# Kernel tuning notes

Hardware: AMD Instinct MI355X
Metric: run time of the kernel (lower is better)

Reference implementation:

```python
import jax, jax.numpy as jnp
import numpy as np

M_POS = 0.5
M_NEG_SIM = 0.1
LAM_NEG = 1.0


def setup_inputs() -> dict:
    key = jax.random.key(0)
    N, d, G = 8192, 1024, 64
    codebook = jax.random.normal(key, (N, d), dtype=jnp.float32)
    base = (jnp.arange(N) // G) * G  # contiguous groups of size G (vq_to_range)
    starts = base.astype(jnp.int32)
    ends = (base + G - 1).astype(jnp.int32)
    return {"codebook": codebook, "starts": starts, "ends": ends, "max_i": N - 1}


def reference(codebook, starts, ends, max_i):
    N, d = codebook.shape
    M = min(N, int(max_i) + 1)  # rows processed by the python loop

    # cosine similarity rows [0:M] vs all N
    zn = codebook / jnp.linalg.norm(codebook, axis=-1, keepdims=True)
    cos = jnp.einsum('md,nd->mn', zn[:M], zn)  # (M, N)

    # pairwise Euclidean distances rows [0:M] vs all N via ||a-b||^2 = |a|^2+|b|^2-2ab
    sq = jnp.sum(codebook * codebook, axis=-1)  # (N,)
    dot = jnp.einsum('md,nd->mn', codebook[:M], codebook)  # (M, N)
    d2 = jnp.maximum(sq[:M, None] + sq[None, :] - 2.0 * dot, 0.0)

    j = jnp.arange(N)[None, :]
    i = jnp.arange(M)[:, None]
    in_range = (j >= starts[:M, None]) & (j <= ends[:M, None])
    pos_mask = in_range & (j != i)
    # original: group_mask[i]=False then neg = ~group_mask, so i is in negatives
    neg_mask = (~in_range) | (j == i)

    pos_cnt = jnp.sum(pos_mask, axis=-1)
    neg_cnt = jnp.sum(neg_mask, axis=-1)

    # safe sqrt: only evaluate on positive-mask entries
    D = jnp.sqrt(jnp.where(pos_mask, d2, 1.0))
    pos_term = jnp.square(jax.nn.relu(D - M_POS)) * pos_mask
    pos_pull = jnp.sum(pos_term, axis=-1) / jnp.maximum(pos_cnt, 1)

    neg_cos = jnp.clip(cos, -1.0, 1.0)
    neg_term = jnp.square(jax.nn.relu(jnp.abs(neg_cos) - M_NEG_SIM)) * neg_mask
    ortho = jnp.sum(neg_term, axis=-1) / jnp.maximum(neg_cnt, 1)

    valid = (pos_cnt > 0) & (neg_cnt > 0)
    per_row = jnp.where(valid, pos_pull + LAM_NEG * ortho, 0.0)
    cnt = jnp.sum(valid)
    total = jnp.sum(per_row)
    return jnp.where(cnt > 0, total / jnp.maximum(cnt, 1).astype(total.dtype), jnp.zeros((), total.dtype))
```

## Files before the change

### kernel.cpp

```cpp
#include <hip/hip_runtime.h>
#include <hip/hip_bf16.h>
#include <stdint.h>

#define M_POS 0.5f
#define M_NEG 0.1f
#define LAM_NEG 1.0f

typedef __attribute__((ext_vector_type(4))) float floatx4;
typedef __attribute__((ext_vector_type(8))) int   intx8;
typedef __attribute__((ext_vector_type(4))) int   int32x4;

union Frag8 { intx8 v; int4 q[2]; };

__global__ __launch_bounds__(256) void prep_kernel(
    const float* __restrict__ cb, unsigned char* __restrict__ cb_q,
    float* __restrict__ sq, float* __restrict__ inv_norm,
    unsigned* __restrict__ zero_base, int zero_len,
    int N, int d)
{
    const int gi = blockIdx.x * 256 + threadIdx.x;
    if (gi < zero_len) zero_base[gi] = 0u;

    const int t = threadIdx.x;
    const int w = t >> 6, l = t & 63;
    const int row = blockIdx.x * 4 + w;
    if (row >= N) return;
    const float* src = cb + (size_t)row * d;
    unsigned char* dst = cb_q + (size_t)row * d;

    float s = 0.f;
    for (int c = l * 16; c < d; c += 1024) {
        float4 v0 = *(const float4*)(src + c);
        float4 v1 = *(const float4*)(src + c + 4);
        float4 v2 = *(const float4*)(src + c + 8);
        float4 v3 = *(const float4*)(src + c + 12);
        s += v0.x*v0.x + v0.y*v0.y + v0.z*v0.z + v0.w*v0.w
           + v1.x*v1.x + v1.y*v1.y + v1.z*v1.z + v1.w*v1.w
           + v2.x*v2.x + v2.y*v2.y + v2.z*v2.z + v2.w*v2.w
           + v3.x*v3.x + v3.y*v3.y + v3.z*v3.z + v3.w*v3.w;
        int p0 = __builtin_amdgcn_cvt_pk_fp8_f32(v0.x, v0.y, 0, false);
        p0     = __builtin_amdgcn_cvt_pk_fp8_f32(v0.z, v0.w, p0, true);
        int p1 = __builtin_amdgcn_cvt_pk_fp8_f32(v1.x, v1.y, 0, false);
        p1     = __builtin_amdgcn_cvt_pk_fp8_f32(v1.z, v1.w, p1, true);
        int p2 = __builtin_amdgcn_cvt_pk_fp8_f32(v2.x, v2.y, 0, false);
        p2     = __builtin_amdgcn_cvt_pk_fp8_f32(v2.z, v2.w, p2, true);
        int p3 = __builtin_amdgcn_cvt_pk_fp8_f32(v3.x, v3.y, 0, false);
        p3     = __builtin_amdgcn_cvt_pk_fp8_f32(v3.z, v3.w, p3, true);
        int32x4 pk; pk.x = p0; pk.y = p1; pk.z = p2; pk.w = p3;
        *(int32x4*)(dst + c) = pk;
    }
    for (int o = 32; o > 0; o >>= 1) s += __shfl_down(s, o, 64);
    if (l == 0) { sq[row] = s; inv_norm[row] = rsqrtf(s); }
}

__global__ __launch_bounds__(512, 1) void gram_loss_kernel(
    const unsigned char* __restrict__ A,
    const float* __restrict__ sq, const float* __restrict__ inv_norm,
    const int* __restrict__ starts, const int* __restrict__ ends,
    const int* __restrict__ max_ip,
    float* __restrict__ pos_acc, float* __restrict__ neg_acc,
    unsigned* __restrict__ counter, float* __restrict__ out,
    int N, int d)
{
    const int M = min(N, max_ip[0] + 1);

    int vt = blockIdx.x;
    const int nB = gridDim.x;
    if ((nB & 7) == 0) {
        const int per = nB >> 3;
        vt = (blockIdx.x & 7) * per + (blockIdx.x >> 3);
    }

    int bx = (int)((sqrtf(8.f * (float)vt + 1.f) - 1.f) * 0.5f);
    while ((bx + 1) * (bx + 2) / 2 <= vt) bx++;
    while (bx * (bx + 1) / 2 > vt) bx--;
    const int by = vt - bx * (bx + 1) / 2;

    const int rowBase = by * 256;
    const int colBase = bx * 256;
    const bool isDiag = (by == bx);

    __shared__ alignas(16) unsigned char ldsA[2][256 * 128];
    __shared__ alignas(16) unsigned char ldsB[2][256 * 128];

    const int tid  = threadIdx.x;
    const int wave = tid >> 6;
    const int lane = tid & 63;
    const int wr = (wave >> 2) * 128;
    const int wc = (wave & 3) * 64;

    floatx4 acc[8][4];
#pragma unroll
    for (int a = 0; a < 8; ++a)
#pragma unroll
        for (int b = 0; b < 4; ++b) acc[a][b] = (floatx4){0.f, 0.f, 0.f, 0.f};

    const int sRow8 = tid >> 3;
    const int sChk  = tid & 7;
    const int srcOffC = ((sChk ^ (sRow8 & 7)) * 16);
    const int kTiles = d / 128;

    const int rl = lane & 15;
    const int g  = lane >> 4;
    const int rx = rl & 7;
    const int c0 = (((2 * g)     ^ rx) * 16);
    const int c1 = (((2 * g + 1) ^ rx) * 16);

#define STAGE(SLOT, KT)                                                         \
    { const int k0_ = (KT) * 128;                                               \
      _Pragma("unroll")                                                         \
      for (int h = 0; h < 4; ++h) {                                             \
        const int r_ = h * 64 + sRow8;                                          \
        const unsigned char* ga_ = A + (size_t)(rowBase + r_) * d + k0_ + srcOffC; \
        const unsigned char* gb_ = A + (size_t)(colBase + r_) * d + k0_ + srcOffC; \
        __builtin_amdgcn_global_load_lds(                                       \
            (const __attribute__((address_space(1))) void*)ga_,                 \
            (__attribute__((address_space(3))) void*)(ldsA[SLOT] + r_ * 128 + sChk * 16), 16, 0, 0); \
        __builtin_amdgcn_global_load_lds(                                       \
            (const __attribute__((address_space(1))) void*)gb_,                 \
            (__attribute__((address_space(3))) void*)(ldsB[SLOT] + r_ * 128 + sChk * 16), 16, 0, 0); \
      } }

#define WAITV(NN)  asm volatile("s_waitcnt vmcnt(" #NN ")" ::: "memory")

    if (kTiles == 8) {
        STAGE(0, 0)
        __builtin_amdgcn_sched_barrier(0);
        STAGE(1, 1)
        __builtin_amdgcn_sched_barrier(0);
#pragma unroll
        for (int kt = 0; kt < 8; ++kt) {
            const int cur = kt & 1;
            if (kt < 7) { WAITV(8); } else { WAITV(0); }
            __builtin_amdgcn_s_barrier();

            Frag8 bfr[4];
#pragma unroll
            for (int ct = 0; ct < 4; ++ct) {
                const unsigned char* pb = ldsB[cur] + (wc + ct * 16 + rl) * 128;
                bfr[ct].q[0] = *(const int4*)(pb + c0);
                bfr[ct].q[1] = *(const int4*)(pb + c1);
            }
#pragma unroll
            for (int ph = 0; ph < 4; ++ph) {
                Frag8 af0, af1;
                const unsigned char* pa0 = ldsA[cur] + (wr + (2 * ph) * 16 + rl) * 128;
                const unsigned char* pa1 = ldsA[cur] + (wr + (2 * ph + 1) * 16 + rl) * 128;
                af0.q[0] = *(const int4*)(pa0 + c0);
                af0.q[1] = *(const int4*)(pa0 + c1);
                af1.q[0] = *(const int4*)(pa1 + c0);
                af1.q[1] = *(const int4*)(pa1 + c1);
                __builtin_amdgcn_s_setprio(1);
#pragma unroll
                for (int ct = 0; ct < 4; ++ct)
                    acc[2 * ph][ct] = __builtin_amdgcn_mfma_scale_f32_16x16x128_f8f6f4(
                        af0.v, bfr[ct].v, acc[2 * ph][ct], 0, 0, 0, 127, 0, 127);
#pragma unroll
                for (int ct = 0; ct < 4; ++ct)
                    acc[2 * ph + 1][ct] = __builtin_amdgcn_mfma_scale_f32_16x16x128_f8f6f4(
                        af1.v, bfr[ct].v, acc[2 * ph + 1][ct], 0, 0, 0, 127, 0, 127);
                __builtin_amdgcn_s_setprio(0);
                __builtin_amdgcn_sched_barrier(0);
            }

            __builtin_amdgcn_s_barrier();
            if (kt + 2 < 8) {
                STAGE(cur, kt + 2)
                __builtin_amdgcn_sched_barrier(0);
            }
        }
    } else {
        for (int kt = 0; kt < kTiles; ++kt) {
            STAGE(0, kt)
            WAITV(0);
            __builtin_amdgcn_s_barrier();
            Frag8 bfr[4];
#pragma unroll
            for (int ct = 0; ct < 4; ++ct) {
                const unsigned char* pb = ldsB[0] + (wc + ct * 16 + rl) * 128;
                bfr[ct].q[0] = *(const int4*)(pb + c0);
                bfr[ct].q[1] = *(const int4*)(pb + c1);
            }
#pragma unroll
            for (int rt = 0; rt < 8; ++rt) {
                Frag8 af;
                const unsigned char* pa = ldsA[0] + (wr + rt * 16 + rl) * 128;
                af.q[0] = *(const int4*)(pa + c0);
                af.q[1] = *(const int4*)(pa + c1);
#pragma unroll
                for (int ct = 0; ct < 4; ++ct)
                    acc[rt][ct] = __builtin_amdgcn_mfma_scale_f32_16x16x128_f8f6f4(
                        af.v, bfr[ct].v, acc[rt][ct], 0, 0, 0, 127, 0, 127);
            }
            __syncthreads();
        }
    }
#undef STAGE
#undef WAITV

    const int q  = lane >> 4;
    const int jlo = colBase + wc;
    const int ilo = rowBase + wr;

    int   jn[4];
    float jinv[4];
    bool  jvalid[4];
#pragma unroll
    for (int ct = 0; ct < 4; ++ct) {
        const int j = jlo + ct * 16 + rl;
        jn[ct]  = j;
        jinv[ct] = inv_norm[j];
        jvalid[ct] = (j < M);
    }

    bool posLane = false;
    {
        const int ri0 = ilo + lane;
        const int ri1 = ilo + 64 + lane;
        if (ri0 < M) posLane |= (ends[ri0] >= jlo) && (starts[ri0] <= jlo + 63);
        if (ri1 < M) posLane |= (ends[ri1] >= jlo) && (starts[ri1] <= jlo + 63);
        if (!isDiag) {
            const int cj = jlo + lane;
            if (cj < M) posLane |= (ends[cj] >= ilo) && (starts[cj] <= ilo + 127);
        }
    }
    const bool fullPath = (__ballot(posLane) != 0ULL);

    float posc[4] = {0.f, 0.f, 0.f, 0.f};
    float negc[4] = {0.f, 0.f, 0.f, 0.f};

    if (fullPath) {
        int   jns[4], jne[4];
        float jsq[4];
#pragma unroll
        for (int ct = 0; ct < 4; ++ct) {
            jsq[ct] = sq[jn[ct]];
            jns[ct] = jvalid[ct] ? starts[jn[ct]] : 0;
            jne[ct] = jvalid[ct] ? ends[jn[ct]]   : -1;
        }
#pragma unroll
        for (int rt = 0; rt < 8; ++rt) {
            const int ibase = ilo + rt * 16 + q * 4;
#pragma unroll
            for (int reg = 0; reg < 4; ++reg) {
                const int i = ibase + reg;
                const bool rowValid = (i < M);
                const int ns = rowValid ? starts[i] : 0;
                const int ne = rowValid ? ends[i]   : -1;
                const float iinv = inv_norm[i];
                const float isq  = sq[i];
                float posp = 0.f, negp = 0.f;
#pragma unroll
                for (int ct = 0; ct < 4; ++ct) {
                    const float dot = acc[rt][ct][reg];
                    const int j = jn[ct];
                    float cosv = dot * iinv * jinv[ct];
                    cosv = fminf(fmaxf(cosv, -1.f), 1.f);
                    float tn = fmaxf(fabsf(cosv) - M_NEG, 0.f);
                    const float nterm = tn * tn;
                    const float d2 = fmaxf(isq + jsq[ct] - 2.f * dot, 0.f);
                    float tp = fmaxf(sqrtf(d2) - M_POS, 0.f);
                    const float pterm = tp * tp;
                    const bool dg = (j == i);
                    if (rowValid) {
                        const bool in_r = (j >= ns) && (j <= ne);
                        if (in_r && !dg) posp += pterm;
                        if (!in_r || dg) negp += nterm;
                    }
                    if (!isDiag && jvalid[ct]) {
                        const bool in_c = (i >= jns[ct]) && (i <= jne[ct]);
                        if (in_c && !dg) posc[ct] += pterm;
                        if (!in_c || dg) negc[ct] += nterm;
                    }
                }
#pragma unroll
                for (int m = 1; m < 16; m <<= 1) {
                    posp += __shfl_xor(posp, m, 64);
                    negp += __shfl_xor(negp, m, 64);
                }
                if (rowValid && rl == 0) {
                    atomicAdd(&pos_acc[i], posp);
                    atomicAdd(&neg_acc[i], negp);
                }
            }
        }
        if (!isDiag) {
#pragma unroll
            for (int ct = 0; ct < 4; ++ct) {
                posc[ct] += __shfl_xor(posc[ct], 16, 64);
                posc[ct] += __shfl_xor(posc[ct], 32, 64);
                negc[ct] += __shfl_xor(negc[ct], 16, 64);
                negc[ct] += __shfl_xor(negc[ct], 32, 64);
            }
            if (q == 0) {
#pragma unroll
                for (int ct = 0; ct < 4; ++ct) {
                    if (jvalid[ct]) {
                        atomicAdd(&pos_acc[jn[ct]], posc[ct]);
                        atomicAdd(&neg_acc[jn[ct]], negc[ct]);
                    }
                }
            }
        }
    } else {
#pragma unroll
        for (int rt = 0; rt < 8; ++rt) {
            const int ibase = ilo + rt * 16 + q * 4;
#pragma unroll
            for (int reg = 0; reg < 4; ++reg) {
                const int i = ibase + reg;
                const float iinv = inv_norm[i];
                float negp = 0.f;
#pragma unroll
                for (int ct = 0; ct < 4; ++ct) {
                    const float dot = acc[rt][ct][reg];
                    float cosv = dot * iinv * jinv[ct];
                    cosv = fminf(fmaxf(cosv, -1.f), 1.f);
                    float tn = fmaxf(fabsf(cosv) - M_NEG, 0.f);
                    const float nterm = tn * tn;
                    negp += nterm;
                    negc[ct] += nterm;
                }
#pragma unroll
                for (int m = 1; m < 16; m <<= 1)
                    negp += __shfl_xor(negp, m, 64);
                if ((i < M) && rl == 0)
                    atomicAdd(&neg_acc[i], negp);
            }
        }
        if (!isDiag) {
#pragma unroll
            for (int ct = 0; ct < 4; ++ct) {
                negc[ct] += __shfl_xor(negc[ct], 16, 64);
                negc[ct] += __shfl_xor(negc[ct], 32, 64);
            }
            if (q == 0) {
#pragma unroll
                for (int ct = 0; ct < 4; ++ct)
                    if (jvalid[ct])
                        atomicAdd(&neg_acc[jn[ct]], negc[ct]);
            }
        }
    }

    struct FinSm { int amLast; float ts[8]; int cs[8]; };
    FinSm* fs = (FinSm*)&ldsA[0][0];
    __syncthreads();
    if (tid == 0) {
        __threadfence();
        unsigned old = atomicAdd(counter, 1u);
        fs->amLast = (old == (unsigned)(gridDim.x - 1)) ? 1 : 0;
    }
    __syncthreads();
    if (fs->amLast) {
        __threadfence();
        float total = 0.f;
        int cnt = 0;
        for (int i = tid; i < M; i += 512) {
            const float pa = __hip_atomic_load(&pos_acc[i], __ATOMIC_RELAXED, __HIP_MEMORY_SCOPE_AGENT);
            const float na = __hip_atomic_load(&neg_acc[i], __ATOMIC_RELAXED, __HIP_MEMORY_SCOPE_AGENT);
            const int ns = starts[i], ne = ends[i];
            const int lo = max(ns, 0), hi = min(ne, N - 1);
            const int inr = max(hi - lo + 1, 0);
            const bool dg = (i >= ns) && (i <= ne);
            const int pos_cnt = inr - (dg ? 1 : 0);
            const int neg_cnt = N - inr + (dg ? 1 : 0);
            if (pos_cnt > 0 && neg_cnt > 0) {
                total += pa / (float)max(pos_cnt, 1)
                       + LAM_NEG * na / (float)max(neg_cnt, 1);
                cnt++;
            }
        }
        for (int o = 32; o > 0; o >>= 1) {
            total += __shfl_down(total, o, 64);
            cnt   += __shfl_down(cnt, o, 64);
        }
        if (lane == 0) { fs->ts[wave] = total; fs->cs[wave] = cnt; }
        __syncthreads();
        if (tid == 0) {
            float T = 0.f; int C = 0;
            for (int wv = 0; wv < 8; ++wv) { T += fs->ts[wv]; C += fs->cs[wv]; }
            out[0] = (C > 0) ? T / (float)C : 0.f;
        }
    }
}

extern "C" void kernel_launch(void* const* d_in, const int* in_sizes, int n_in,
                              void* d_out, int out_size, void* d_ws, size_t ws_size,
                              hipStream_t stream) {
    const float* cb     = (const float*)d_in[0];
    const int*   starts = (const int*)d_in[1];
    const int*   ends   = (const int*)d_in[2];
    const int*   max_ip = (const int*)d_in[3];
    float* out = (float*)d_out;

    const int N = in_sizes[1];
    const int d = in_sizes[0] / N;

    char* ws = (char*)d_ws;
    unsigned char* cb_q = (unsigned char*)ws;
    size_t off = ((size_t)N * d + 255) & ~(size_t)255;
    float* sq       = (float*)(ws + off); off += (size_t)N * 4;
    float* inv_norm = (float*)(ws + off); off += (size_t)N * 4;
    float* pos_acc  = (float*)(ws + off); off += (size_t)N * 4;
    float* neg_acc  = (float*)(ws + off); off += (size_t)N * 4;
    unsigned* counter = (unsigned*)(ws + off); off += 256;

    prep_kernel<<<(N + 3) / 4, 256, 0, stream>>>(cb, cb_q, sq, inv_norm,
                                                 (unsigned*)pos_acc, 2 * N + 1, N, d);

    const int nb = N / 256;
    const int nBlocks = nb * (nb + 1) / 2;
    gram_loss_kernel<<<nBlocks, 512, 0, stream>>>(cb_q, sq, inv_norm, starts, ends,
                                                  max_ip, pos_acc, neg_acc, counter,
                                                  out, N, d);
}
```

Measured before the change: 202.4 us.

## Interleave next-tile global-to-LDS prefetches between MFMA phases with barrier ping-pong

Splits the tile staging into separate A and B half-stages. They are issued between the four MFMA phases of each k-tile, instead of as one burst after all compute. Each phase now reads its A fragments, waits on lgkmcnt, and runs its MFMAs under raised priority, with workgroup barriers around it. The aim is to overlap global loads with matrix math and keep LDS reads off the MFMA critical path. The cost is several extra s_barriers per k-tile and a tighter ordering of LDS slot reuse.

```diff
diff --git a/kernel.cpp b/kernel.cpp
--- a/kernel.cpp
+++ b/kernel.cpp
@@ -106,72 +106,113 @@
     const int c0 = (((2 * g)     ^ rx) * 16);
     const int c1 = (((2 * g + 1) ^ rx) * 16);
 
-#define STAGE(SLOT, KT)                                                         \
-    { const int k0_ = (KT) * 128;                                               \
+#define STAGE_A(SLOT, KT, H)                                                    \
+    { const int r_ = (H) * 64 + sRow8;                                          \
+      const unsigned char* ga_ = A + (size_t)(rowBase + r_) * d + (KT) * 128 + srcOffC; \
+      __builtin_amdgcn_global_load_lds(                                         \
+          (const __attribute__((address_space(1))) void*)ga_,                   \
+          (__attribute__((address_space(3))) void*)(ldsA[SLOT] + r_ * 128 + sChk * 16), 16, 0, 0); }
+
+#define STAGE_B(SLOT, KT, H)                                                    \
+    { const int r_ = (H) * 64 + sRow8;                                          \
+      const unsigned char* gb_ = A + (size_t)(colBase + r_) * d + (KT) * 128 + srcOffC; \
+      __builtin_amdgcn_global_load_lds(                                         \
+          (const __attribute__((address_space(1))) void*)gb_,                   \
+          (__attribute__((address_space(3))) void*)(ldsB[SLOT] + r_ * 128 + sChk * 16), 16, 0, 0); }
+
+#define WAITV(NN)   asm volatile("s_waitcnt vmcnt(" #NN ")" ::: "memory")
+#define WAITLGKM0   asm volatile("s_waitcnt lgkmcnt(0)" ::: "memory")
+#define SBAR        __builtin_amdgcn_s_barrier()
+#define SCHED0      __builtin_amdgcn_sched_barrier(0)
+
+#define READ_A2(AF0, AF1, CUR, ROFF)                                            \
+    { const unsigned char* pa0_ = ldsA[CUR] + (wr + (ROFF)      + rl) * 128;    \
+      const unsigned char* pa1_ = ldsA[CUR] + (wr + (ROFF) + 16 + rl) * 128;    \
+      AF0.q[0] = *(const int4*)(pa0_ + c0);  AF0.q[1] = *(const int4*)(pa0_ + c1); \
+      AF1.q[0] = *(const int4*)(pa1_ + c0);  AF1.q[1] = *(const int4*)(pa1_ + c1); }
+
+#define MFMA8(AF0, AF1, R0)                                                     \
+    { _Pragma("unroll")                                                         \
+      for (int ct = 0; ct < 4; ++ct)                                            \
+          acc[R0][ct] = __builtin_amdgcn_mfma_scale_f32_16x16x128_f8f6f4(       \
+              AF0.v, bfr[ct].v, acc[R0][ct], 0, 0, 0, 127, 0, 127);             \
       _Pragma("unroll")                                                         \
-      for (int h = 0; h < 4; ++h) {                                             \
-        const int r_ = h * 64 + sRow8;                                          \
-        const unsigned char* ga_ = A + (size_t)(rowBase + r_) * d + k0_ + srcOffC; \
-        const unsigned char* gb_ = A + (size_t)(colBase + r_) * d + k0_ + srcOffC; \
-        __builtin_amdgcn_global_load_lds(                                       \
-            (const __attribute__((address_space(1))) void*)ga_,                 \
-            (__attribute__((address_space(3))) void*)(ldsA[SLOT] + r_ * 128 + sChk * 16), 16, 0, 0); \
-        __builtin_amdgcn_global_load_lds(                                       \
-            (const __attribute__((address_space(1))) void*)gb_,                 \
-            (__attribute__((address_space(3))) void*)(ldsB[SLOT] + r_ * 128 + sChk * 16), 16, 0, 0); \
-      } }
-
-#define WAITV(NN)  asm volatile("s_waitcnt vmcnt(" #NN ")" ::: "memory")
+      for (int ct = 0; ct < 4; ++ct)                                            \
+          acc[(R0) + 1][ct] = __builtin_amdgcn_mfma_scale_f32_16x16x128_f8f6f4( \
+              AF1.v, bfr[ct].v, acc[(R0) + 1][ct], 0, 0, 0, 127, 0, 127); }
 
     if (kTiles == 8) {
-        STAGE(0, 0)
-        __builtin_amdgcn_sched_barrier(0);
-        STAGE(1, 1)
-        __builtin_amdgcn_sched_barrier(0);
+#pragma unroll
+        for (int h = 0; h < 4; ++h) { STAGE_A(0, 0, h) STAGE_B(0, 0, h) }
+        SCHED0;
+#pragma unroll
+        for (int h = 0; h < 4; ++h) { STAGE_A(1, 1, h) STAGE_B(1, 1, h) }
+        SCHED0;
+
 #pragma unroll
         for (int kt = 0; kt < 8; ++kt) {
             const int cur = kt & 1;
             if (kt < 7) { WAITV(8); } else { WAITV(0); }
-            __builtin_amdgcn_s_barrier();
+            SBAR;
 
             Frag8 bfr[4];
+            Frag8 af0, af1;
+
 #pragma unroll
             for (int ct = 0; ct < 4; ++ct) {
                 const unsigned char* pb = ldsB[cur] + (wc + ct * 16 + rl) * 128;
                 bfr[ct].q[0] = *(const int4*)(pb + c0);
                 bfr[ct].q[1] = *(const int4*)(pb + c1);
             }
-#pragma unroll
-            for (int ph = 0; ph < 4; ++ph) {
-                Frag8 af0, af1;
-                const unsigned char* pa0 = ldsA[cur] + (wr + (2 * ph) * 16 + rl) * 128;
-                const unsigned char* pa1 = ldsA[cur] + (wr + (2 * ph + 1) * 16 + rl) * 128;
-                af0.q[0] = *(const int4*)(pa0 + c0);
-                af0.q[1] = *(const int4*)(pa0 + c1);
-                af1.q[0] = *(const int4*)(pa1 + c0);
-                af1.q[1] = *(const int4*)(pa1 + c1);
-                __builtin_amdgcn_s_setprio(1);
-#pragma unroll
-                for (int ct = 0; ct < 4; ++ct)
-                    acc[2 * ph][ct] = __builtin_amdgcn_mfma_scale_f32_16x16x128_f8f6f4(
-                        af0.v, bfr[ct].v, acc[2 * ph][ct], 0, 0, 0, 127, 0, 127);
-#pragma unroll
-                for (int ct = 0; ct < 4; ++ct)
-                    acc[2 * ph + 1][ct] = __builtin_amdgcn_mfma_scale_f32_16x16x128_f8f6f4(
-                        af1.v, bfr[ct].v, acc[2 * ph + 1][ct], 0, 0, 0, 127, 0, 127);
-                __builtin_amdgcn_s_setprio(0);
-                __builtin_amdgcn_sched_barrier(0);
-            }
-
-            __builtin_amdgcn_s_barrier();
+            READ_A2(af0, af1, cur, 0)
+            SBAR;
+            WAITLGKM0; SCHED0;
+            __builtin_amdgcn_s_setprio(1);
+            MFMA8(af0, af1, 0)
+            __builtin_amdgcn_s_setprio(0);
+            SCHED0;
+            SBAR;
+
+            READ_A2(af0, af1, cur, 32)
             if (kt + 2 < 8) {
-                STAGE(cur, kt + 2)
-                __builtin_amdgcn_sched_barrier(0);
-            }
+#pragma unroll
+                for (int h = 0; h < 4; ++h) STAGE_B(cur, kt + 2, h)
+            }
+            SCHED0;
+            SBAR;
+            WAITLGKM0; SCHED0;
+            __builtin_amdgcn_s_setprio(1);
+            MFMA8(af0, af1, 2)
+            __builtin_amdgcn_s_setprio(0);
+            SCHED0;
+            SBAR;
+
+            READ_A2(af0, af1, cur, 64)
+            if (kt + 2 < 8) { STAGE_A(cur, kt + 2, 0) STAGE_A(cur, kt + 2, 2) }
+            SCHED0;
+            SBAR;
+            WAITLGKM0; SCHED0;
+            __builtin_amdgcn_s_setprio(1);
+            MFMA8(af0, af1, 4)
+            __builtin_amdgcn_s_setprio(0);
+            SCHED0;
+            SBAR;
+
+            READ_A2(af0, af1, cur, 96)
+            SBAR;
+            WAITLGKM0; SCHED0;
+            __builtin_amdgcn_s_setprio(1);
+            MFMA8(af0, af1, 6)
+            __builtin_amdgcn_s_setprio(0);
+            SCHED0;
+            SBAR;
+
+            if (kt + 2 < 8) { STAGE_A(cur, kt + 2, 1) STAGE_A(cur, kt + 2, 3) SCHED0; }
         }
     } else {
         for (int kt = 0; kt < kTiles; ++kt) {
-            STAGE(0, kt)
+#pragma unroll
+            for (int h = 0; h < 4; ++h) { STAGE_A(0, kt, h) STAGE_B(0, kt, h) }
             WAITV(0);
             __builtin_amdgcn_s_barrier();
             Frag8 bfr[4];
@@ -182,21 +223,23 @@
                 bfr[ct].q[1] = *(const int4*)(pb + c1);
             }
 #pragma unroll
-            for (int rt = 0; rt < 8; ++rt) {
-                Frag8 af;
-                const unsigned char* pa = ldsA[0] + (wr + rt * 16 + rl) * 128;
-                af.q[0] = *(const int4*)(pa + c0);
-                af.q[1] = *(const int4*)(pa + c1);
-#pragma unroll
-                for (int ct = 0; ct < 4; ++ct)
-                    acc[rt][ct] = __builtin_amdgcn_mfma_scale_f32_16x16x128_f8f6f4(
-                        af.v, bfr[ct].v, acc[rt][ct], 0, 0, 0, 127, 0, 127);
+            for (int rt = 0; rt < 8; rt += 2) {
+                Frag8 af0, af1;
+                READ_A2(af0, af1, 0, rt * 16)
+                WAITLGKM0; SCHED0;
+                MFMA8(af0, af1, rt)
             }
             __syncthreads();
         }
     }
-#undef STAGE
+#undef STAGE_A
+#undef STAGE_B
 #undef WAITV
+#undef WAITLGKM0
+#undef SBAR
+#undef SCHED0
+#undef READ_A2
+#undef MFMA8
 
     const int q  = lane >> 4;
     const int jlo = colBase + wc;
```

After: 200.4 us (median of 2 runs). About the same (-1.0%).

## Skip duplicate B loads on diagonal tiles and remap tile order for L2 locality

Applied to the files above, without the earlier changes.

On diagonal tiles the B operand is the same rows as A, so the B global-to-LDS copy is skipped and the B fragments are read from the A buffer, with the vmcnt wait adjusted to match. For N=8192 a new blocked enumeration of the upper-triangular tiles groups them into super-tiles so that concurrently running blocks share rows, which should improve L2 reuse. The unrolled 8-k-tile pipeline is replaced by a generic double-buffered loop over kTiles, which may lose some of the hand-tuned scheduling. The new tile decode is a serial loop per block and adds a little startup cost.

```diff
diff --git a/kernel.cpp b/kernel.cpp
--- a/kernel.cpp
+++ b/kernel.cpp
@@ -71,10 +71,36 @@
         vt = (blockIdx.x & 7) * per + (blockIdx.x >> 3);
     }
 
-    int bx = (int)((sqrtf(8.f * (float)vt + 1.f) - 1.f) * 0.5f);
-    while ((bx + 1) * (bx + 2) / 2 <= vt) bx++;
-    while (bx * (bx + 1) / 2 > vt) bx--;
-    const int by = vt - bx * (bx + 1) / 2;
+    int by = -1, bx = -1;
+    const int nb = N / 256;
+    if (nb == 32) {
+        int rem = vt;
+        for (int bxs = 0; bxs < 8 && by < 0; ++bxs) {
+            const int hi = bxs * 4 + 3;
+            for (int bys = 0; bys <= (bxs >> 1) && by < 0; ++bys) {
+                int cnt = 0;
+#pragma unroll
+                for (int r = 0; r < 8; ++r) {
+                    const int byy = bys * 8 + r;
+                    const int lo = max(byy, bxs * 4);
+                    cnt += max(0, hi - lo + 1);
+                }
+                if (rem >= cnt) { rem -= cnt; continue; }
+                for (int r = 0; r < 8; ++r) {
+                    const int byy = bys * 8 + r;
+                    const int lo = max(byy, bxs * 4);
+                    const int c = max(0, hi - lo + 1);
+                    if (rem < c) { by = byy; bx = lo + rem; break; }
+                    rem -= c;
+                }
+            }
+        }
+    } else {
+        bx = (int)((sqrtf(8.f * (float)vt + 1.f) - 1.f) * 0.5f);
+        while ((bx + 1) * (bx + 2) / 2 <= vt) bx++;
+        while (bx * (bx + 1) / 2 > vt) bx--;
+        by = vt - bx * (bx + 1) / 2;
+    }
 
     const int rowBase = by * 256;
     const int colBase = bx * 256;
@@ -112,79 +138,51 @@
       for (int h = 0; h < 4; ++h) {                                             \
         const int r_ = h * 64 + sRow8;                                          \
         const unsigned char* ga_ = A + (size_t)(rowBase + r_) * d + k0_ + srcOffC; \
-        const unsigned char* gb_ = A + (size_t)(colBase + r_) * d + k0_ + srcOffC; \
         __builtin_amdgcn_global_load_lds(                                       \
             (const __attribute__((address_space(1))) void*)ga_,                 \
             (__attribute__((address_space(3))) void*)(ldsA[SLOT] + r_ * 128 + sChk * 16), 16, 0, 0); \
-        __builtin_amdgcn_global_load_lds(                                       \
-            (const __attribute__((address_space(1))) void*)gb_,                 \
-            (__attribute__((address_space(3))) void*)(ldsB[SLOT] + r_ * 128 + sChk * 16), 16, 0, 0); \
+      }                                                                         \
+      if (!isDiag) {                                                            \
+        _Pragma("unroll")                                                       \
+        for (int h = 0; h < 4; ++h) {                                           \
+          const int r_ = h * 64 + sRow8;                                        \
+          const unsigned char* gb_ = A + (size_t)(colBase + r_) * d + k0_ + srcOffC; \
+          __builtin_amdgcn_global_load_lds(                                     \
+              (const __attribute__((address_space(1))) void*)gb_,               \
+              (__attribute__((address_space(3))) void*)(ldsB[SLOT] + r_ * 128 + sChk * 16), 16, 0, 0); \
+        }                                                                       \
       } }
 
 #define WAITV(NN)  asm volatile("s_waitcnt vmcnt(" #NN ")" ::: "memory")
 
-    if (kTiles == 8) {
+    {
         STAGE(0, 0)
         __builtin_amdgcn_sched_barrier(0);
         STAGE(1, 1)
         __builtin_amdgcn_sched_barrier(0);
-#pragma unroll
-        for (int kt = 0; kt < 8; ++kt) {
+
+        for (int kt = 0; kt < kTiles; ++kt) {
             const int cur = kt & 1;
-            if (kt < 7) { WAITV(8); } else { WAITV(0); }
+            if (kt < kTiles - 1) {
+                if (isDiag) { WAITV(4); } else { WAITV(8); }
+            } else {
+                WAITV(0);
+            }
             __builtin_amdgcn_s_barrier();
 
+            const unsigned char* bbase = isDiag ? ldsA[cur] : ldsB[cur];
             Frag8 bfr[4];
 #pragma unroll
             for (int ct = 0; ct < 4; ++ct) {
-                const unsigned char* pb = ldsB[cur] + (wc + ct * 16 + rl) * 128;
+                const unsigned char* pb = bbase + (wc + ct * 16 + rl) * 128;
                 bfr[ct].q[0] = *(const int4*)(pb + c0);
                 bfr[ct].q[1] = *(const int4*)(pb + c1);
             }
-#pragma unroll
-            for (int ph = 0; ph < 4; ++ph) {
-                Frag8 af0, af1;
-                const unsigned char* pa0 = ldsA[cur] + (wr + (2 * ph) * 16 + rl) * 128;
-                const unsigned char* pa1 = ldsA[cur] + (wr + (2 * ph + 1) * 16 + rl) * 128;
-                af0.q[0] = *(const int4*)(pa0 + c0);
-                af0.q[1] = *(const int4*)(pa0 + c1);
-                af1.q[0] = *(const int4*)(pa1 + c0);
-                af1.q[1] = *(const int4*)(pa1 + c1);
-                __builtin_amdgcn_s_setprio(1);
-#pragma unroll
-                for (int ct = 0; ct < 4; ++ct)
-                    acc[2 * ph][ct] = __builtin_amdgcn_mfma_scale_f32_16x16x128_f8f6f4(
-                        af0.v, bfr[ct].v, acc[2 * ph][ct], 0, 0, 0, 127, 0, 127);
-#pragma unroll
-                for (int ct = 0; ct < 4; ++ct)
-                    acc[2 * ph + 1][ct] = __builtin_amdgcn_mfma_scale_f32_16x16x128_f8f6f4(
-                        af1.v, bfr[ct].v, acc[2 * ph + 1][ct], 0, 0, 0, 127, 0, 127);
-                __builtin_amdgcn_s_setprio(0);
-                __builtin_amdgcn_sched_barrier(0);
-            }
-
-            __builtin_amdgcn_s_barrier();
-            if (kt + 2 < 8) {
-                STAGE(cur, kt + 2)
-                __builtin_amdgcn_sched_barrier(0);
-            }
-        }
-    } else {
-        for (int kt = 0; kt < kTiles; ++kt) {
-            STAGE(0, kt)
-            WAITV(0);
-            __builtin_amdgcn_s_barrier();
-            Frag8 bfr[4];
-#pragma unroll
-            for (int ct = 0; ct < 4; ++ct) {
-                const unsigned char* pb = ldsB[0] + (wc + ct * 16 + rl) * 128;
-                bfr[ct].q[0] = *(const int4*)(pb + c0);
-                bfr[ct].q[1] = *(const int4*)(pb + c1);
-            }
+            __builtin_amdgcn_s_setprio(1);
 #pragma unroll
             for (int rt = 0; rt < 8; ++rt) {
                 Frag8 af;
-                const unsigned char* pa = ldsA[0] + (wr + rt * 16 + rl) * 128;
+                const unsigned char* pa = ldsA[cur] + (wr + rt * 16 + rl) * 128;
                 af.q[0] = *(const int4*)(pa + c0);
                 af.q[1] = *(const int4*)(pa + c1);
 #pragma unroll
@@ -192,7 +190,14 @@
                     acc[rt][ct] = __builtin_amdgcn_mfma_scale_f32_16x16x128_f8f6f4(
                         af.v, bfr[ct].v, acc[rt][ct], 0, 0, 0, 127, 0, 127);
             }
-            __syncthreads();
+            __builtin_amdgcn_s_setprio(0);
+            __builtin_amdgcn_sched_barrier(0);
+
+            __builtin_amdgcn_s_barrier();
+            if (kt + 2 < kTiles) {
+                STAGE(cur, kt + 2)
+                __builtin_amdgcn_sched_barrier(0);
+            }
         }
     }
 #undef STAGE
```

Result: slower. 220.5 us (+9.0%).
